# Optimization experiments

Hardware: AMD Instinct MI355X
Metric: run time of the kernel (lower is better)

The kernel has to match this reference:

```python
import jax, jax.numpy as jnp
import numpy as np

CONF_THRES = 0.96
IOU_THRES = 0.45
MAX_CAND = 2048        # fixed candidate cap (jit-static stand-in for data-dependent nonzero)
DET_PER_IMG = 300
AGNOSTIC = False
LABEL_OFF = 4.0        # class offset for batched NMS; boxes lie within [-0.5, 1.5]


def _cxcywh_to_xyxy(b):
    cx, cy, w, h = b[..., 0], b[..., 1], b[..., 2], b[..., 3]
    return jnp.stack([cx - 0.5 * w, cy - 0.5 * h, cx + 0.5 * w, cy + 0.5 * h], axis=-1)


def _box_iou(a, b):
    # a: [K,4], b: [K,4] -> [K,K]
    lt = jnp.maximum(a[:, None, :2], b[None, :, :2])
    rb = jnp.minimum(a[:, None, 2:], b[None, :, 2:])
    wh = jnp.clip(rb - lt, 0.0)
    inter = wh[..., 0] * wh[..., 1]
    area_a = (a[:, 2] - a[:, 0]) * (a[:, 3] - a[:, 1])
    area_b = (b[:, 2] - b[:, 0]) * (b[:, 3] - b[:, 1])
    return inter / (area_a[:, None] + area_b[None, :] - inter + 1e-9)


def _process_image(x, nc):
    # x: [N, 5+nc]
    obj = x[:, 4]
    cls_scores = x[:, 5:] * obj[:, None]                 # x[:,5:] *= x[:,4:5]
    boxes = _cxcywh_to_xyxy(x[:, :4])                    # [N,4]
    # multi-label candidates: (obj > conf) pre-filter, then (obj*cls > conf)
    cand_mask = (cls_scores > CONF_THRES) & (obj[:, None] > CONF_THRES)
    flat_scores = jnp.where(cand_mask, cls_scores, -1.0).reshape(-1)  # [N*nc]
    top_scores, top_idx = jax.lax.top_k(flat_scores, MAX_CAND)        # sorted desc
    anchor = top_idx // nc
    label = top_idx % nc
    cand_boxes = boxes[anchor]                           # [K,4]
    valid = top_scores > 0.0

    # batched (class-aware) NMS via per-class coordinate offset
    if AGNOSTIC:
        nms_boxes = cand_boxes
    else:
        nms_boxes = cand_boxes + (label.astype(cand_boxes.dtype) * LABEL_OFF)[:, None]
    iou = _box_iou(nms_boxes, nms_boxes)                 # [K,K]
    idxs = jnp.arange(MAX_CAND)

    def body(i, keep):
        suppress = keep[i] & (iou[i] > IOU_THRES) & (idxs > i)
        return keep & ~suppress

    keep = jax.lax.fori_loop(0, MAX_CAND, body, valid)
    kept_scores = jnp.where(keep, top_scores, -1.0)
    det_scores, det_idx = jax.lax.top_k(kept_scores, DET_PER_IMG)
    det_valid = det_scores > 0.0
    det = jnp.concatenate(
        [cand_boxes[det_idx], det_scores[:, None], label[det_idx].astype(x.dtype)[:, None]],
        axis=1,
    )  # [DET_PER_IMG, 6] = (x1, y1, x2, y2, score, class)
    return jnp.where(det_valid[:, None], det, 0.0)


def setup_inputs() -> dict:
    key = jax.random.key(0)
    prediction = jax.random.uniform(key, (8, 25200, 85), dtype=jnp.float32)
    return {"prediction": prediction}


def reference(prediction):
    nc = prediction.shape[2] - 5
    return jax.vmap(lambda x: _process_image(x, nc))(prediction)
```

## Files before the change

### kernel.cpp

```cpp
#include <hip/hip_runtime.h>
#include <stdint.h>

#define CONF 0.96f
#define IOUT 0.45f
#define NA 25200
#define DIM 85
#define NC 80
#define NIMG 8
#define NCAND 2048
#define CAPRAW 4096
#define NDET 300
#define CSTRIDE 32

__global__ void k0_zero(int* __restrict__ cnt) {
    cnt[threadIdx.x] = 0;
}

#define APB 112
#define BCAP 256
__global__ __launch_bounds__(256) void k1_filter(
    const float* __restrict__ pred, int* __restrict__ cnt,
    float* __restrict__ raw_s, int* __restrict__ raw_f) {
    __shared__ float lds[APB * DIM];
    __shared__ float l_s[BCAP];
    __shared__ int   l_f[BCAP];
    __shared__ int   l_cnt, l_base;
    int tid = threadIdx.x;
    int img = blockIdx.y;
    int a0 = blockIdx.x * APB;
    if (tid == 0) l_cnt = 0;

    const float4* src = (const float4*)(pred + ((size_t)img * NA + a0) * DIM);
    float4* dst = (float4*)lds;
    for (int i = tid; i < (APB * DIM / 4); i += 256) dst[i] = src[i];
    __syncthreads();

    for (int it = 0; it < (APB * NC / 256); ++it) {
        int w = tid + it * 256;
        int al = w / NC;
        int c = w - al * NC;
        float obj = lds[al * DIM + 4];
        float s = lds[al * DIM + 5 + c] * obj;
        if (s > CONF && obj > CONF) {
            int p = atomicAdd(&l_cnt, 1);
            if (p < BCAP) { l_s[p] = s; l_f[p] = (a0 + al) * NC + c; }
        }
    }
    __syncthreads();
    int c = l_cnt; if (c > BCAP) c = BCAP;
    if (tid == 0) l_base = c ? atomicAdd(&cnt[img * CSTRIDE], c) : 0;
    __syncthreads();
    int base = l_base;
    for (int i = tid; i < c; i += 256) {
        int pos = base + i;
        if (pos < CAPRAW) {
            raw_s[img * CAPRAW + pos] = l_s[i];
            raw_f[img * CAPRAW + pos] = l_f[i];
        }
    }
}

__global__ __launch_bounds__(256) void k2_rank(
    const float* __restrict__ pred,
    const int* __restrict__ cnt, int* __restrict__ n_arr,
    const float* __restrict__ raw_s, const int* __restrict__ raw_f,
    float* __restrict__ score, int* __restrict__ label,
    float* __restrict__ ox1, float* __restrict__ oy1,
    float* __restrict__ ox2, float* __restrict__ oy2,
    float* __restrict__ area,
    float* __restrict__ rx1, float* __restrict__ ry1,
    float* __restrict__ rx2, float* __restrict__ ry2) {
    __shared__ uint64_t keys[CAPRAW];
    int img = blockIdx.y;
    int tid = threadIdx.x;
    int m = cnt[img * CSTRIDE]; if (m > CAPRAW) m = CAPRAW;
    if (blockIdx.x == 0 && tid == 0) n_arr[img] = m < NCAND ? m : NCAND;

    const float* rs = raw_s + img * CAPRAW;
    const int*   rf = raw_f + img * CAPRAW;
    for (int j = tid; j < CAPRAW; j += 256) {
        uint64_t k = 0;
        if (j < m)
            k = ((uint64_t)__float_as_uint(rs[j]) << 32) | (uint32_t)(~(uint32_t)rf[j]);
        keys[j] = k;
    }
    __syncthreads();
    if (blockIdx.x * 256 >= m) return;

    int idx = blockIdx.x * 256 + tid;
    bool valid = idx < m;
    uint64_t my = keys[idx];
    int mt = (m + 7) & ~7;
    int rank = 0;
#pragma unroll 8
    for (int j = 0; j < mt; ++j) rank += (keys[j] > my) ? 1 : 0;

    if (valid && rank < NCAND) {
        float s = __uint_as_float((uint32_t)(my >> 32));
        uint32_t myf = ~((uint32_t)my);
        int anchor = (int)(myf / NC);
        int lab = (int)(myf - (uint32_t)anchor * NC);
        const float* p = pred + ((size_t)img * NA + anchor) * DIM;
        float cx = p[0], cy = p[1], wv = p[2], hv = p[3];
        float x1 = cx - 0.5f * wv, y1 = cy - 0.5f * hv;
        float x2 = cx + 0.5f * wv, y2 = cy + 0.5f * hv;
        float off = (float)lab * 4.0f;
        size_t o = (size_t)img * NCAND + rank;
        score[o] = s; label[o] = lab;
        rx1[o] = x1; ry1[o] = y1; rx2[o] = x2; ry2[o] = y2;
        float o1 = x1 + off, o2 = y1 + off, o3 = x2 + off, o4 = y2 + off;
        ox1[o] = o1; oy1[o] = o2; ox2[o] = o3; oy2[o] = o4;
        area[o] = (o3 - o1) * (o4 - o2);
    }
}

#define ITILE 32
__global__ __launch_bounds__(256) void k3_mask(
    const int* __restrict__ n_arr,
    const float* __restrict__ ox1, const float* __restrict__ oy1,
    const float* __restrict__ ox2, const float* __restrict__ oy2,
    const float* __restrict__ area, uint32_t* __restrict__ mask) {
    __shared__ float4 jb[NCAND];
    __shared__ float  ja[NCAND];
    int img = blockIdx.y;
    int n = n_arr[img];
    int tid = threadIdx.x;
    size_t base = (size_t)img * NCAND;
    for (int j = tid; j < NCAND; j += 256) {
        float4 v = make_float4(0.f, 0.f, 0.f, 0.f);
        float ar = 0.f;
        if (j < n) {
            v = make_float4(ox1[base + j], oy1[base + j], ox2[base + j], oy2[base + j]);
            ar = area[base + j];
        }
        jb[j] = v; ja[j] = ar;
    }
    __syncthreads();

    int lane = tid & 63, wv = tid >> 6;
    int i0 = blockIdx.x * ITILE + wv * (ITILE / 4);
    for (int ii = 0; ii < ITILE / 4; ++ii) {
        int i = i0 + ii;
        float4 a = jb[i];
        float aar = ja[i];
        uint32_t word = 0;
#pragma unroll
        for (int b = 0; b < 32; ++b) {
            int j = lane + (b << 6);
            float4 bb = jb[j];
            float bar = ja[j];
            float ltx = fmaxf(a.x, bb.x), lty = fmaxf(a.y, bb.y);
            float rbx = fminf(a.z, bb.z), rby = fminf(a.w, bb.w);
            float w2 = fmaxf(rbx - ltx, 0.0f), h2 = fmaxf(rby - lty, 0.0f);
            float inter = w2 * h2;
            float iou = inter / (aar + bar - inter + 1e-9f);
            word |= (iou > IOUT && j > i) ? (1u << b) : 0u;
        }
        mask[(base + i) * 64 + lane] = word;
    }
}

__global__ void k4_scan(const int* __restrict__ n_arr,
                        const uint32_t* __restrict__ mask,
                        const float* __restrict__ score, const int* __restrict__ label,
                        const float* __restrict__ rx1, const float* __restrict__ ry1,
                        const float* __restrict__ rx2, const float* __restrict__ ry2,
                        float* __restrict__ out) {
    int img = blockIdx.x;
    int lane = threadIdx.x;
    int n = n_arr[img];
    size_t cbase = (size_t)img * NCAND;
    const uint32_t* rowp = mask + cbase * 64 + lane;
    float* outp = out + (size_t)img * NDET * 6;

    uint32_t removed = 0;
    int kcnt = 0;
    constexpr int PF = 32;
    uint32_t buf[PF];
#pragma unroll
    for (int k = 0; k < PF; ++k) buf[k] = rowp[(size_t)k * 64];
    for (int ib = 0; ib < n; ib += PF) {
#pragma unroll
        for (int k = 0; k < PF; ++k) {
            int i = ib + k;
            uint32_t row = buf[k];
            int pi = i + PF; if (pi > NCAND - 1) pi = NCAND - 1;
            buf[k] = rowp[(size_t)pi * 64];
            uint32_t w = (uint32_t)__builtin_amdgcn_readlane((int)removed, i & 63);
            uint32_t kept = ((w >> (i >> 6)) & 1u) ^ 1u;
            kcnt += (int)kept;
            removed |= row & (0u - kept);
        }
        if (kcnt >= NDET) break;
    }

    int bsum = 0;
    for (int b = 0; b < 32; ++b) {
        int j = lane + (b << 6);
        bool kept = (j < n) && (((removed >> b) & 1u) == 0u);
        unsigned long long m64 = __ballot(kept);
        if (kept) {
            int r = bsum + (int)__popcll(m64 & ((1ull << lane) - 1ull));
            if (r < NDET) {
                float* o = outp + (size_t)r * 6;
                o[0] = rx1[cbase + j]; o[1] = ry1[cbase + j];
                o[2] = rx2[cbase + j]; o[3] = ry2[cbase + j];
                o[4] = score[cbase + j]; o[5] = (float)label[cbase + j];
            }
        }
        bsum += (int)__popcll(m64);
        if (bsum >= NDET) break;
    }
    int nk = bsum < NDET ? bsum : NDET;
    for (int idx = nk * 6 + lane; idx < NDET * 6; idx += 64) outp[idx] = 0.0f;
}

extern "C" void kernel_launch(void* const* d_in, const int* in_sizes, int n_in,
                              void* d_out, int out_size, void* d_ws, size_t ws_size,
                              hipStream_t stream) {
    const float* pred = (const float*)d_in[0];
    float* out = (float*)d_out;
    char* w = (char*)d_ws;

    const size_t A_CNT = 0;
    const size_t A_N   = 1024;
    const size_t A_RS  = 1280;
    const size_t SZ_RAW = (size_t)NIMG * CAPRAW * 4;
    const size_t A_RF  = A_RS + SZ_RAW;
    const size_t SA    = A_RF + SZ_RAW;
    const size_t SZ_S  = (size_t)NIMG * NCAND * 4;

    int*   cnt   = (int*)(w + A_CNT);
    int*   n_arr = (int*)(w + A_N);
    float* raw_s = (float*)(w + A_RS);
    int*   raw_f = (int*)(w + A_RF);
    float* score = (float*)(w + SA + 0 * SZ_S);
    int*   label = (int*)(w + SA + 1 * SZ_S);
    float* ox1   = (float*)(w + SA + 2 * SZ_S);
    float* oy1   = (float*)(w + SA + 3 * SZ_S);
    float* ox2   = (float*)(w + SA + 4 * SZ_S);
    float* oy2   = (float*)(w + SA + 5 * SZ_S);
    float* area  = (float*)(w + SA + 6 * SZ_S);
    float* rx1   = (float*)(w + SA + 7 * SZ_S);
    float* ry1   = (float*)(w + SA + 8 * SZ_S);
    float* rx2   = (float*)(w + SA + 9 * SZ_S);
    float* ry2   = (float*)(w + SA + 10 * SZ_S);
    uint32_t* mask = (uint32_t*)(w + SA + 11 * SZ_S);

    k0_zero<<<1, NIMG * CSTRIDE, 0, stream>>>(cnt);
    dim3 g1(NA / APB, NIMG);
    k1_filter<<<g1, 256, 0, stream>>>(pred, cnt, raw_s, raw_f);
    dim3 g2(CAPRAW / 256, NIMG);
    k2_rank<<<g2, 256, 0, stream>>>(pred, cnt, n_arr, raw_s, raw_f,
        score, label, ox1, oy1, ox2, oy2, area, rx1, ry1, rx2, ry2);
    dim3 g3(NCAND / ITILE, NIMG);
    k3_mask<<<g3, 256, 0, stream>>>(n_arr, ox1, oy1, ox2, oy2, area, mask);
    k4_scan<<<NIMG, 64, 0, stream>>>(n_arr, mask, score, label,
        rx1, ry1, rx2, ry2, out);
}
```

Baseline: 193.3 us.

## Tile IoU mask by upper-triangular 64x64 chunk pairs and skip empty candidate chunks

Replaces the dense IoU mask kernel with one that launches only upper-triangular 64x64 tile pairs and exits early when the row chunk lies beyond the valid candidate count. The mask layout changes to contiguous 64-bit words per row, and the scan kernel's bit indexing and final compaction are adapted to it, using a prefix-sum compaction in place of ballot loops. The mask buffer is now zeroed with a memset so skipped tiles read as no suppression. This adds a large memset and many tiny 64-thread blocks in exchange for avoiding lower-triangle and out-of-range IoU work.

```diff
diff --git a/kernel.cpp b/kernel.cpp
--- a/kernel.cpp
+++ b/kernel.cpp
@@ -11,10 +11,9 @@
 #define CAPRAW 4096
 #define NDET 300
 #define CSTRIDE 32
-
-__global__ void k0_zero(int* __restrict__ cnt) {
-    cnt[threadIdx.x] = 0;
-}
+#define CH 64
+#define NCH (NCAND / CH)
+#define NTPAIR ((NCH * (NCH + 1)) / 2)
 
 #define APB 112
 #define BCAP 256
@@ -114,50 +113,48 @@
     }
 }
 
-#define ITILE 32
-__global__ __launch_bounds__(256) void k3_mask(
+__global__ __launch_bounds__(64) void k3_mask(
     const int* __restrict__ n_arr,
     const float* __restrict__ ox1, const float* __restrict__ oy1,
     const float* __restrict__ ox2, const float* __restrict__ oy2,
-    const float* __restrict__ area, uint32_t* __restrict__ mask) {
-    __shared__ float4 jb[NCAND];
-    __shared__ float  ja[NCAND];
+    const float* __restrict__ area, uint64_t* __restrict__ mask64) {
     int img = blockIdx.y;
     int n = n_arr[img];
-    int tid = threadIdx.x;
+    int p = blockIdx.x, ci = 0;
+    while (p >= NCH - ci) { p -= NCH - ci; ++ci; }
+    int cj = ci + p;
+    if (ci * CH >= n) return;
+    int t = threadIdx.x;
     size_t base = (size_t)img * NCAND;
-    for (int j = tid; j < NCAND; j += 256) {
-        float4 v = make_float4(0.f, 0.f, 0.f, 0.f);
-        float ar = 0.f;
+    __shared__ float jx1[CH], jy1[CH], jx2[CH], jy2[CH], jar[CH];
+    {
+        int j = cj * CH + t;
+        float x1 = 0.f, y1 = 0.f, x2 = 0.f, y2 = 0.f, ar = 0.f;
         if (j < n) {
-            v = make_float4(ox1[base + j], oy1[base + j], ox2[base + j], oy2[base + j]);
-            ar = area[base + j];
-        }
-        jb[j] = v; ja[j] = ar;
-    }
-    __syncthreads();
-
-    int lane = tid & 63, wv = tid >> 6;
-    int i0 = blockIdx.x * ITILE + wv * (ITILE / 4);
-    for (int ii = 0; ii < ITILE / 4; ++ii) {
-        int i = i0 + ii;
-        float4 a = jb[i];
-        float aar = ja[i];
-        uint32_t word = 0;
-#pragma unroll
-        for (int b = 0; b < 32; ++b) {
-            int j = lane + (b << 6);
-            float4 bb = jb[j];
-            float bar = ja[j];
-            float ltx = fmaxf(a.x, bb.x), lty = fmaxf(a.y, bb.y);
-            float rbx = fminf(a.z, bb.z), rby = fminf(a.w, bb.w);
-            float w2 = fmaxf(rbx - ltx, 0.0f), h2 = fmaxf(rby - lty, 0.0f);
-            float inter = w2 * h2;
-            float iou = inter / (aar + bar - inter + 1e-9f);
-            word |= (iou > IOUT && j > i) ? (1u << b) : 0u;
-        }
-        mask[(base + i) * 64 + lane] = word;
-    }
+            x1 = ox1[base + j]; y1 = oy1[base + j];
+            x2 = ox2[base + j]; y2 = oy2[base + j]; ar = area[base + j];
+        }
+        jx1[t] = x1; jy1[t] = y1; jx2[t] = x2; jy2[t] = y2; jar[t] = ar;
+    }
+    __syncthreads();
+    int i = ci * CH + t;
+    float ax1 = 0.f, ay1 = 0.f, ax2 = 0.f, ay2 = 0.f, aar = 0.f;
+    if (i < n) {
+        ax1 = ox1[base + i]; ay1 = oy1[base + i];
+        ax2 = ox2[base + i]; ay2 = oy2[base + i]; aar = area[base + i];
+    }
+    int jg0 = cj * CH;
+    uint64_t w = 0;
+#pragma unroll 8
+    for (int jj = 0; jj < CH; ++jj) {
+        float ltx = fmaxf(ax1, jx1[jj]), lty = fmaxf(ay1, jy1[jj]);
+        float rbx = fminf(ax2, jx2[jj]), rby = fminf(ay2, jy2[jj]);
+        float ww = fmaxf(rbx - ltx, 0.f), hh = fmaxf(rby - lty, 0.f);
+        float inter = ww * hh;
+        float iou = inter / (aar + jar[jj] - inter + 1e-9f);
+        w |= (iou > IOUT && (jg0 + jj) > i) ? (1ull << jj) : 0ull;
+    }
+    mask64[(base + (size_t)i) * NCH + cj] = w;
 }
 
 __global__ void k4_scan(const int* __restrict__ n_arr,
@@ -186,32 +183,39 @@
             uint32_t row = buf[k];
             int pi = i + PF; if (pi > NCAND - 1) pi = NCAND - 1;
             buf[k] = rowp[(size_t)pi * 64];
-            uint32_t w = (uint32_t)__builtin_amdgcn_readlane((int)removed, i & 63);
-            uint32_t kept = ((w >> (i >> 6)) & 1u) ^ 1u;
+            uint32_t w = (uint32_t)__builtin_amdgcn_readlane((int)removed, i >> 5);
+            uint32_t kept = ((w >> (i & 31)) & 1u) ^ 1u;
             kcnt += (int)kept;
             removed |= row & (0u - kept);
         }
         if (kcnt >= NDET) break;
     }
 
-    int bsum = 0;
-    for (int b = 0; b < 32; ++b) {
-        int j = lane + (b << 6);
-        bool kept = (j < n) && (((removed >> b) & 1u) == 0u);
-        unsigned long long m64 = __ballot(kept);
-        if (kept) {
-            int r = bsum + (int)__popcll(m64 & ((1ull << lane) - 1ull));
-            if (r < NDET) {
-                float* o = outp + (size_t)r * 6;
-                o[0] = rx1[cbase + j]; o[1] = ry1[cbase + j];
-                o[2] = rx2[cbase + j]; o[3] = ry2[cbase + j];
-                o[4] = score[cbase + j]; o[5] = (float)label[cbase + j];
-            }
-        }
-        bsum += (int)__popcll(m64);
-        if (bsum >= NDET) break;
-    }
-    int nk = bsum < NDET ? bsum : NDET;
+    int j0 = lane << 5;
+    uint32_t vmask = (j0 + 32 <= n) ? 0xffffffffu
+                   : (j0 >= n ? 0u : ((1u << (n - j0)) - 1u));
+    uint32_t keptw = ~removed & vmask;
+    int cnt = __popc(keptw);
+    int pre = cnt;
+    for (int d = 1; d < 64; d <<= 1) {
+        int tv = __shfl_up(pre, d);
+        if (lane >= d) pre += tv;
+    }
+    int total = __shfl(pre, 63);
+    int r = pre - cnt;
+    uint32_t wv = keptw;
+    while (wv) {
+        int b = __builtin_ctz(wv);
+        wv &= wv - 1;
+        if (r >= NDET) break;
+        int j = j0 + b;
+        float* o = outp + (size_t)r * 6;
+        o[0] = rx1[cbase + j]; o[1] = ry1[cbase + j];
+        o[2] = rx2[cbase + j]; o[3] = ry2[cbase + j];
+        o[4] = score[cbase + j]; o[5] = (float)label[cbase + j];
+        ++r;
+    }
+    int nk = total < NDET ? total : NDET;
     for (int idx = nk * 6 + lane; idx < NDET * 6; idx += 64) outp[idx] = 0.0f;
 }
 
@@ -245,16 +249,18 @@
     float* ry1   = (float*)(w + SA + 8 * SZ_S);
     float* rx2   = (float*)(w + SA + 9 * SZ_S);
     float* ry2   = (float*)(w + SA + 10 * SZ_S);
-    uint32_t* mask = (uint32_t*)(w + SA + 11 * SZ_S);
-
-    k0_zero<<<1, NIMG * CSTRIDE, 0, stream>>>(cnt);
+    uint64_t* mask64 = (uint64_t*)(w + SA + 11 * SZ_S);
+    uint32_t* mask32 = (uint32_t*)mask64;
+
+    hipMemsetAsync(cnt, 0, NIMG * CSTRIDE * sizeof(int), stream);
+    hipMemsetAsync(mask64, 0, (size_t)NIMG * NCAND * NCH * 8, stream);
     dim3 g1(NA / APB, NIMG);
     k1_filter<<<g1, 256, 0, stream>>>(pred, cnt, raw_s, raw_f);
     dim3 g2(CAPRAW / 256, NIMG);
     k2_rank<<<g2, 256, 0, stream>>>(pred, cnt, n_arr, raw_s, raw_f,
         score, label, ox1, oy1, ox2, oy2, area, rx1, ry1, rx2, ry2);
-    dim3 g3(NCAND / ITILE, NIMG);
-    k3_mask<<<g3, 256, 0, stream>>>(n_arr, ox1, oy1, ox2, oy2, area, mask);
-    k4_scan<<<NIMG, 64, 0, stream>>>(n_arr, mask, score, label,
+    dim3 g3(NTPAIR, NIMG);
+    k3_mask<<<g3, CH, 0, stream>>>(n_arr, ox1, oy1, ox2, oy2, area, mask64);
+    k4_scan<<<NIMG, 64, 0, stream>>>(n_arr, mask32, score, label,
         rx1, ry1, rx2, ry2, out);
 }
```

After: 180.1 us. -6.9%, faster.
